# Optimization experiments

Measured on AMD Instinct MI355X. Metric: run time of the kernel, lower is better.

The kernel has to match this reference:

```python
import jax, jax.numpy as jnp
import numpy as np

D = 512          # hidden_dim
H_HEADS = 8
DH = D // H_HEADS  # 64
L = 6            # n_layers
P = 8            # patch size
KT = 3           # temporal kernel
Z_DIM = 32
FILM_SCALE = 0.5
ROPE_BASE = 10000.0
EPS = 1e-5


def layer_norm(x, g, b):
    mu = x.mean(-1, keepdims=True)
    var = ((x - mu) ** 2).mean(-1, keepdims=True)
    return (x - mu) * jax.lax.rsqrt(var + EPS) * g + b


def rotate_half(x):
    x1, x2 = jnp.split(x, 2, axis=-1)
    return jnp.concatenate([-x2, x1], axis=-1)


def rope_time(T, dtype):
    half = DH // 2
    inv_freq = ROPE_BASE ** (-(jnp.arange(half, dtype=dtype) / half))  # (half,)
    angles = jnp.arange(T, dtype=dtype)[:, None] * inv_freq[None, :]   # (T, half)
    sin = jnp.concatenate([jnp.sin(angles), jnp.sin(angles)], -1)      # (T, DH)
    cos = jnp.concatenate([jnp.cos(angles), jnp.cos(angles)], -1)
    return sin, cos


def setup_inputs() -> dict:
    key = jax.random.key(0)
    ks = iter(jax.random.split(key, 64))
    n = lambda shape, s=0.02: jax.random.normal(next(ks), shape, jnp.float32) * s
    inp = {
        "x": jax.random.normal(next(ks), (16, 32, 3, 64, 64), jnp.float32),
        "z": jax.random.normal(next(ks), (16, 32, Z_DIM), jnp.float32),
        # tokenizer: CausalConv3d (kt,ph,pw)=(3,8,8), stride (1,8,8)
        "conv_w": n((D, 3, KT, P, P)),
        "conv_b": jnp.zeros((D,), jnp.float32),
        "tok_g": jnp.ones((D,), jnp.float32),
        "tok_b": jnp.zeros((D,), jnp.float32),
        # FiLM from z -> (gamma, beta)
        "film_w": n((Z_DIM, 2 * D)),
        "film_b": jnp.zeros((2 * D,), jnp.float32),
        # transformer blocks (stacked over L)
        "ln1_g": jnp.ones((L, D), jnp.float32), "ln1_b": jnp.zeros((L, D), jnp.float32),
        "kqv_w": n((L, D, 3 * D)), "kqv_b": jnp.zeros((L, 3 * D), jnp.float32),
        "proj_w": n((L, D, D)), "proj_b": jnp.zeros((L, D), jnp.float32),
        "ln2_g": jnp.ones((L, D), jnp.float32), "ln2_b": jnp.zeros((L, D), jnp.float32),
        "mlp_w1": n((L, D, 4 * D)), "mlp_b1": jnp.zeros((L, 4 * D), jnp.float32),
        "mlp_w2": n((L, 4 * D, D)), "mlp_b2": jnp.zeros((L, D), jnp.float32),
        "rs_attn": jnp.full((L,), 0.5, jnp.float32),
        "rs_mlp": jnp.full((L,), 0.5, jnp.float32),
        # scoring head
        "head_g": jnp.ones((D,), jnp.float32), "head_b": jnp.zeros((D,), jnp.float32),
        "head_w": n((D, 1)), "head_bias": jnp.zeros((1,), jnp.float32),
    }
    return inp


def _forward(x, z, conv_w, conv_b, tok_g, tok_b, film_w, film_b,
             ln1_g, ln1_b, kqv_w, kqv_b, proj_w, proj_b, ln2_g, ln2_b,
             mlp_w1, mlp_b1, mlp_w2, mlp_b2, rs_attn, rs_mlp,
             head_g, head_b, head_w, head_bias):
    B, T, C, Himg, Wimg = x.shape
    # ---- SpatialTemporalTokenizer: causal Conv3d (pad time on past only) ----
    xc = jnp.transpose(x, (0, 2, 1, 3, 4))  # [B,C,T,H,W]
    y = jax.lax.conv_general_dilated(
        xc, conv_w, window_strides=(1, P, P),
        padding=[(KT - 1, 0), (0, 0), (0, 0)],
        dimension_numbers=("NCDHW", "OIDHW", "NCDHW"))
    y = y + conv_b[None, :, None, None, None]          # [B,D,T,Hn,Wn]
    Hn, Wn = y.shape[3], y.shape[4]
    tok = jnp.transpose(y, (0, 2, 3, 4, 1)).reshape(B, T, Hn * Wn, D)
    tok = layer_norm(tok, tok_g, tok_b)                 # [B,T,N,D]
    # ---- FiLM conditioning from z ----
    gb = z @ film_w + film_b                            # [B,T,2D]
    gamma, beta = jnp.split(gb, 2, axis=-1)
    tok = (1.0 + FILM_SCALE * gamma)[:, :, None, :] * tok + (FILM_SCALE * beta)[:, :, None, :]
    # ---- spatial pooling -> temporal sequence ----
    h = tok.mean(axis=2)                                # [B,T,D]
    # ---- transformer stack (causal, time RoPE, pre-LN, gated residuals) ----
    sin_t, cos_t = rope_time(T, h.dtype)                # (T, DH)
    causal = jnp.tril(jnp.ones((T, T), bool))
    neg_inf = jnp.finfo(h.dtype).min
    for i in range(L):
        xi = layer_norm(h, ln1_g[i], ln1_b[i])
        kqv = xi @ kqv_w[i] + kqv_b[i]                  # [B,T,3D]
        k, q, v = jnp.split(kqv, 3, axis=-1)            # torch chunk order: k,q,v
        sh = lambda t: t.reshape(B, T, H_HEADS, DH).transpose(0, 2, 1, 3)  # [B,h,T,d]
        q, k, v = sh(q), sh(k), sh(v)
        q = q * cos_t + rotate_half(q) * sin_t
        k = k * cos_t + rotate_half(k) * sin_t
        att = jnp.einsum("bhqd,bhkd->bhqk", q, k) / np.sqrt(DH)
        att = jnp.where(causal[None, None], att, neg_inf)
        att = jax.nn.softmax(att, axis=-1)
        yv = jnp.einsum("bhqk,bhkd->bhqd", att, v)
        yv = yv.transpose(0, 2, 1, 3).reshape(B, T, D)
        attn_out = yv @ proj_w[i] + proj_b[i]
        h = h + rs_attn[i] * attn_out
        x2 = layer_norm(h, ln2_g[i], ln2_b[i])
        m = jax.nn.gelu(x2 @ mlp_w1[i] + mlp_b1[i], approximate=False) @ mlp_w2[i] + mlp_b2[i]
        h = h + rs_mlp[i] * m
    # ---- per-timestep score head ----
    h = layer_norm(h, head_g, head_b)
    score = (h @ head_w + head_bias)[..., 0]            # [B,T]
    return score


def reference(x, z, conv_w, conv_b, tok_g, tok_b, film_w, film_b,
              ln1_g, ln1_b, kqv_w, kqv_b, proj_w, proj_b, ln2_g, ln2_b,
              mlp_w1, mlp_b1, mlp_w2, mlp_b2, rs_attn, rs_mlp,
              head_g, head_b, head_w, head_bias):
    return _forward(x, z, conv_w, conv_b, tok_g, tok_b, film_w, film_b,
                    ln1_g, ln1_b, kqv_w, kqv_b, proj_w, proj_b, ln2_g, ln2_b,
                    mlp_w1, mlp_b1, mlp_w2, mlp_b2, rs_attn, rs_mlp,
                    head_g, head_b, head_w, head_bias)
```

## Files before the change

### kernel.cpp

```cpp
#include <hip/hip_runtime.h>
#include <math.h>

#define EPS 1e-5f

typedef __attribute__((ext_vector_type(8))) short short8;
typedef __attribute__((ext_vector_type(4))) float f32x4;

__device__ __forceinline__ short f2bf(float f) {
    unsigned u = __float_as_uint(f);
    u += 0x7fffu + ((u >> 16) & 1u);
    return (short)(u >> 16);
}
__device__ __forceinline__ float bf2f(short s) {
    return __uint_as_float(((unsigned)(unsigned short)s) << 16);
}
__device__ __forceinline__ void async16(const void* g, void* l) {
    __builtin_amdgcn_global_load_lds(
        (const __attribute__((address_space(1))) unsigned*)g,
        (__attribute__((address_space(3))) unsigned*)l, 16, 0, 0);
}

__device__ __forceinline__ float block_reduce_sum_256(float v, float* red) {
    #pragma unroll
    for (int o = 32; o > 0; o >>= 1) v += __shfl_down(v, o, 64);
    __syncthreads();
    if ((threadIdx.x & 63) == 0) red[threadIdx.x >> 6] = v;
    __syncthreads();
    return red[0] + red[1] + red[2] + red[3];
}

__global__ __launch_bounds__(256) void prep_all(
    const float* __restrict__ z, const float* __restrict__ fw,
    const float* __restrict__ fb, float* __restrict__ gb,
    const float* __restrict__ conv_w, short* __restrict__ wbf,
    const float* __restrict__ x, short* __restrict__ xbf,
    float* __restrict__ ropeS, float* __restrict__ ropeC,
    const float* __restrict__ kqv_w, short* __restrict__ kqvT,
    const float* __restrict__ proj_w, short* __restrict__ projT,
    const float* __restrict__ mlp_w1, short* __restrict__ mlp1T,
    const float* __restrict__ mlp_w2, short* __restrict__ mlp2T) {
    int bi = blockIdx.x, tid = threadIdx.x;
    if (bi < 512) {
        __shared__ float zs[32];
        if (tid < 32) zs[tid] = z[bi * 32 + tid];
        __syncthreads();
        for (int j = tid; j < 1024; j += 256) {
            float acc = fb[j];
            #pragma unroll
            for (int k = 0; k < 32; k++) acc = fmaf(zs[k], fw[k * 1024 + j], acc);
            gb[bi * 1024 + j] = acc;
        }
        return;
    }
    if (bi < 1664) {
        int i = (bi - 512) * 256 + tid;
        wbf[i] = f2bf(conv_w[i]);
        return;
    }
    if (bi < 4736) {
        int i = (bi - 1664) * 256 + tid;
        float4 a = *(const float4*)(x + (size_t)i * 8);
        float4 b = *(const float4*)(x + (size_t)i * 8 + 4);
        short8 o = {f2bf(a.x), f2bf(a.y), f2bf(a.z), f2bf(a.w),
                    f2bf(b.x), f2bf(b.y), f2bf(b.z), f2bf(b.w)};
        *(short8*)(xbf + (size_t)i * 8) = o;
        return;
    }
    if (bi < 4740) {
        int idx = (bi - 4736) * 256 + tid;
        if (idx < 1024) {
            int t = idx >> 5, j = idx & 31;
            float ang = (float)t * expf(-(float)j * (logf(10000.f) / 32.f));
            ropeS[idx] = sinf(ang);
            ropeC[idx] = cosf(ang);
        }
        return;
    }
    __shared__ float tile[32][33];
    int rel0 = bi - 4740;
    const float* src; short* dst; int NT, K, N, rel;
    if (rel0 < 4608)       { src = kqv_w;  dst = kqvT;  NT = 48; K = 512;  N = 1536; rel = rel0; }
    else if (rel0 < 6144)  { src = proj_w; dst = projT; NT = 16; K = 512;  N = 512;  rel = rel0 - 4608; }
    else if (rel0 < 12288) { src = mlp_w1; dst = mlp1T; NT = 64; K = 512;  N = 2048; rel = rel0 - 6144; }
    else                   { src = mlp_w2; dst = mlp2T; NT = 16; K = 2048; N = 512;  rel = rel0 - 12288; }
    int per = NT * (K / 32);
    int layer = rel / per, r2 = rel - layer * per;
    int nt = r2 % NT, kt = r2 / NT;
    src += (size_t)layer * K * N;
    dst += (size_t)layer * N * K;
    int n0 = nt * 32, k0 = kt * 32;
    int lx = tid & 31, ly = tid >> 5;
    #pragma unroll
    for (int i = 0; i < 32; i += 8)
        tile[ly + i][lx] = src[(size_t)(k0 + ly + i) * N + n0 + lx];
    __syncthreads();
    int kp = tid & 15, nn = tid >> 4;
    #pragma unroll
    for (int i = 0; i < 2; i++) {
        int row = nn + i * 16;
        short2 o = {f2bf(tile[kp * 2][row]), f2bf(tile[kp * 2 + 1][row])};
        *(short2*)(dst + (size_t)(n0 + row) * K + k0 + kp * 2) = o;
    }
}

__global__ __launch_bounds__(256, 2) void conv_fused(
    const short* __restrict__ xbf, const short* __restrict__ wbf,
    const float* __restrict__ cb, const float* __restrict__ tg,
    const float* __restrict__ tb, const float* __restrict__ gb,
    float* __restrict__ h) {
    __shared__ short As[64 * 32];
    __shared__ short Bs[512 * 32];
    __shared__ float redsum[4][64], redss[4][64];
    __shared__ float mu_s[64], inv_s[64];
    int bt = blockIdx.x, b = bt >> 5, t = bt & 31;
    int tid = threadIdx.x;
    int wave = tid >> 6, lane = tid & 63, quad = lane >> 4, l16 = lane & 15;

    int rowA = tid >> 2;
    int cA = (tid & 3) ^ ((rowA >> 1) & 3);
    int hn = rowA >> 3, wn2 = rowA & 7;
    long long baseA = (((long long)(b * 32 + t - 2) * 3) << 12)
                      + (long long)(hn * 8) * 64 + wn2 * 8;

    f32x4 acc[4][8];
    #pragma unroll
    for (int mt = 0; mt < 4; mt++)
        #pragma unroll
        for (int nt = 0; nt < 8; nt++) acc[mt][nt] = (f32x4){0.f, 0.f, 0.f, 0.f};

    for (int k0 = 0; k0 < 576; k0 += 32) {
        #pragma unroll
        for (int e = 0; e < 8; e++) {
            int s = e * 256 + tid;
            int n = s >> 2;
            int c = (s & 3) ^ ((n >> 1) & 3);
            async16(wbf + (size_t)n * 576 + k0 + c * 8, Bs + s * 8);
        }
        {
            int ks = (k0 >> 3) + cA;
            int ch = (ks >= 24) + (ks >= 48);
            int r = ks - ch * 24;
            int kt = r >> 3, ph = r & 7;
            short8 v8 = (short8){0, 0, 0, 0, 0, 0, 0, 0};
            if (t + kt >= 2)
                v8 = *(const short8*)(xbf + baseA
                        + ((long long)(kt * 3 + ch) << 12) + ph * 64);
            *(short8*)(As + tid * 8) = v8;
        }
        __syncthreads();
        short8 af[4], bf[8];
        #pragma unroll
        for (int mt = 0; mt < 4; mt++) {
            int row = mt * 16 + l16;
            int pc = quad ^ ((row >> 1) & 3);
            af[mt] = *(const short8*)(As + row * 32 + pc * 8);
        }
        #pragma unroll
        for (int nt = 0; nt < 8; nt++) {
            int row = wave * 128 + nt * 16 + l16;
            int pc = quad ^ ((row >> 1) & 3);
            bf[nt] = *(const short8*)(Bs + row * 32 + pc * 8);
        }
        #pragma unroll
        for (int mt = 0; mt < 4; mt++)
            #pragma unroll
            for (int nt = 0; nt < 8; nt++)
                acc[mt][nt] = __builtin_amdgcn_mfma_f32_16x16x32_bf16(
                    af[mt], bf[nt], acc[mt][nt], 0, 0, 0);
        __syncthreads();
    }

    float cbn[8], tgn[8], tbn[8], Gn[8], Ben[8];
    #pragma unroll
    for (int nt = 0; nt < 8; nt++) {
        int n = wave * 128 + nt * 16 + l16;
        cbn[nt] = cb[n]; tgn[nt] = tg[n]; tbn[nt] = tb[n];
        Gn[nt]  = 1.f + 0.5f * gb[bt * 1024 + n];
        Ben[nt] = 0.5f * gb[bt * 1024 + 512 + n];
    }
    #pragma unroll
    for (int mt = 0; mt < 4; mt++)
        #pragma unroll
        for (int reg = 0; reg < 4; reg++) {
            float s = 0.f, ss = 0.f;
            #pragma unroll
            for (int nt = 0; nt < 8; nt++) {
                float v = acc[mt][nt][reg] + cbn[nt];
                s += v; ss += v * v;
            }
            #pragma unroll
            for (int o = 1; o < 16; o <<= 1) {
                s  += __shfl_xor(s, o, 64);
                ss += __shfl_xor(ss, o, 64);
            }
            if (l16 == 0) {
                int m = mt * 16 + quad * 4 + reg;
                redsum[wave][m] = s; redss[wave][m] = ss;
            }
        }
    __syncthreads();
    if (tid < 64) {
        float S  = redsum[0][tid] + redsum[1][tid] + redsum[2][tid] + redsum[3][tid];
        float SS = redss[0][tid] + redss[1][tid] + redss[2][tid] + redss[3][tid];
        float mu = S * (1.f / 512.f);
        float var = SS * (1.f / 512.f) - mu * mu;
        mu_s[tid] = mu; inv_s[tid] = rsqrtf(var + EPS);
    }
    __syncthreads();
    float hacc[8] = {0.f, 0.f, 0.f, 0.f, 0.f, 0.f, 0.f, 0.f};
    #pragma unroll
    for (int mt = 0; mt < 4; mt++)
        #pragma unroll
        for (int reg = 0; reg < 4; reg++) {
            int m = mt * 16 + quad * 4 + reg;
            float mu = mu_s[m], inv = inv_s[m];
            #pragma unroll
            for (int nt = 0; nt < 8; nt++) {
                float v = acc[mt][nt][reg] + cbn[nt];
                hacc[nt] += (v - mu) * inv;
            }
        }
    #pragma unroll
    for (int nt = 0; nt < 8; nt++) {
        hacc[nt] += __shfl_xor(hacc[nt], 16, 64);
        hacc[nt] += __shfl_xor(hacc[nt], 32, 64);
    }
    if (quad == 0)
        #pragma unroll
        for (int nt = 0; nt < 8; nt++) {
            int n = wave * 128 + nt * 16 + l16;
            h[bt * 512 + n] = Gn[nt] * (tgn[nt] * (hacc[nt] * (1.f / 64.f)) + tbn[nt])
                              + Ben[nt];
        }
}

__global__ __launch_bounds__(256) void attn_fused(
    const float* __restrict__ hsrc, const float* __restrict__ lng,
    const float* __restrict__ lnb, const short* __restrict__ Bw,
    const float* __restrict__ bias, const float* __restrict__ ropeS,
    const float* __restrict__ ropeC, short* __restrict__ yv) {
    __shared__ char smem[57344] __attribute__((aligned(16)));
    __shared__ float mu_s[32], inv_s[32];
    short* As = (short*)smem;
    short* Bs = (short*)(smem + 32768);
    float (*qsf)[64] = (float(*)[64])(smem);
    float (*ksf)[64] = (float(*)[64])(smem + 8192);
    short* vT  = (short*)(smem + 16384);
    short* qrb = (short*)(smem + 20480);
    short* krb = (short*)(smem + 24576);
    float (*att)[33] = (float(*)[33])(smem + 28672);
    short* pA  = (short*)(smem + 36864);
    int blk = blockIdx.x, b = blk >> 3, hh = blk & 7;
    int tid = threadIdx.x;
    int m0 = b * 32;
    {
        int row = tid >> 3, l8 = tid & 7;
        const float* hp = hsrc + (size_t)(m0 + row) * 512 + l8 * 64;
        float s = 0.f, ss = 0.f;
        #pragma unroll
        for (int i = 0; i < 16; i++) {
            float4 v = *(const float4*)(hp + i * 4);
            s += v.x + v.y + v.z + v.w;
            ss += v.x * v.x + v.y * v.y + v.z * v.z + v.w * v.w;
        }
        s += __shfl_xor(s, 1, 64); ss += __shfl_xor(ss, 1, 64);
        s += __shfl_xor(s, 2, 64); ss += __shfl_xor(ss, 2, 64);
        s += __shfl_xor(s, 4, 64); ss += __shfl_xor(ss, 4, 64);
        if (l8 == 0) {
            float mu = s * (1.f / 512.f);
            float var = ss * (1.f / 512.f) - mu * mu;
            mu_s[row] = mu;
            inv_s[row] = rsqrtf(var + EPS);
        }
    }
    __syncthreads();
    #pragma unroll
    for (int e = 0; e < 8; e++) {
        int lc = e * 256 + tid;
        int row = lc >> 6, cc = lc & 63;
        float mu = mu_s[row], inv = inv_s[row];
        const float* hp = hsrc + (size_t)(m0 + row) * 512 + cc * 8;
        float4 a = *(const float4*)hp, b2 = *(const float4*)(hp + 4);
        float4 g0 = *(const float4*)(lng + cc * 8), g1 = *(const float4*)(lng + cc * 8 + 4);
        float4 b0 = *(const float4*)(lnb + cc * 8), b1 = *(const float4*)(lnb + cc * 8 + 4);
        short8 o = {f2bf((a.x - mu) * inv * g0.x + b0.x),
                    f2bf((a.y - mu) * inv * g0.y + b0.y),
                    f2bf((a.z - mu) * inv * g0.z + b0.z),
                    f2bf((a.w - mu) * inv * g0.w + b0.w),
                    f2bf((b2.x - mu) * inv * g1.x + b1.x),
                    f2bf((b2.y - mu) * inv * g1.y + b1.y),
                    f2bf((b2.z - mu) * inv * g1.z + b1.z),
                    f2bf((b2.w - mu) * inv * g1.w + b1.w)};
        *(short8*)(As + (row * 64 + (cc ^ (row & 7))) * 8) = o;
    }
    __syncthreads();
    int wave = tid >> 6, lane = tid & 63, quad = lane >> 4, l16 = lane & 15;
    f32x4 acc[2][3];
    #pragma unroll
    for (int m2 = 0; m2 < 2; m2++)
        #pragma unroll
        for (int g = 0; g < 3; g++) acc[m2][g] = (f32x4){0.f, 0.f, 0.f, 0.f};
    for (int k0 = 0; k0 < 512; k0 += 64) {
        #pragma unroll
        for (int e = 0; e < 6; e++) {
            int p = e * 256 + tid;
            int row = p >> 3, seg = (p & 7) ^ (row & 7);
            int n = ((row >> 6) << 9) + hh * 64 + (row & 63);
            async16(Bw + (size_t)n * 512 + k0 + seg * 8, Bs + p * 8);
        }
        __syncthreads();
        #pragma unroll
        for (int ksub = 0; ksub < 2; ksub++) {
            int ccb = ksub * 4 + quad;
            short8 af[2], bf[3];
            #pragma unroll
            for (int m2 = 0; m2 < 2; m2++) {
                int row = m2 * 16 + l16;
                int cc = (k0 >> 3) + ccb;
                af[m2] = *(const short8*)(As + (row * 64 + (cc ^ (row & 7))) * 8);
            }
            #pragma unroll
            for (int g = 0; g < 3; g++) {
                int row = g * 64 + wave * 16 + l16;
                bf[g] = *(const short8*)(Bs + (row * 8 + (ccb ^ (row & 7))) * 8);
            }
            #pragma unroll
            for (int m2 = 0; m2 < 2; m2++)
                #pragma unroll
                for (int g = 0; g < 3; g++)
                    acc[m2][g] = __builtin_amdgcn_mfma_f32_16x16x32_bf16(
                        af[m2], bf[g], acc[m2][g], 0, 0, 0);
        }
        __syncthreads();
    }
    float bb0 = bias[hh * 64 + wave * 16 + l16];
    float bb1 = bias[512 + hh * 64 + wave * 16 + l16];
    float bb2 = bias[1024 + hh * 64 + wave * 16 + l16];
    int dcol = wave * 16 + l16;
    #pragma unroll
    for (int m2 = 0; m2 < 2; m2++)
        #pragma unroll
        for (int reg = 0; reg < 4; reg++) {
            int tkn = m2 * 16 + quad * 4 + reg;
            ksf[tkn][dcol] = acc[m2][0][reg] + bb0;
            qsf[tkn][dcol] = acc[m2][1][reg] + bb1;
            vT[dcol * 32 + (((tkn >> 3) ^ (dcol & 3)) << 3) + (tkn & 7)]
                = f2bf(acc[m2][2][reg] + bb2);
        }
    __syncthreads();
    #pragma unroll
    for (int e = 0; e < 8; e++) {
        int idx = e * 256 + tid;
        int t = idx >> 6, d = idx & 63, j = d & 31;
        float sv = ropeS[t * 32 + j], cv = ropeC[t * 32 + j];
        float qv = qsf[t][d], kv = ksf[t][d];
        float qo = qsf[t][d ^ 32], ko = ksf[t][d ^ 32];
        float rq = (d < 32) ? -qo : qo;
        float rk = (d < 32) ? -ko : ko;
        int addr = t * 64 + (((d >> 3) ^ (t & 7)) << 3) + (d & 7);
        qrb[addr] = f2bf(qv * cv + rq * sv);
        krb[addr] = f2bf(kv * cv + rk * sv);
    }
    __syncthreads();
    int mw = wave & 1, nw = wave >> 1;
    {
        f32x4 sc = (f32x4){0.f, 0.f, 0.f, 0.f};
        #pragma unroll
        for (int kc = 0; kc < 2; kc++) {
            int rq = mw * 16 + l16;
            int rk = nw * 16 + l16;
            short8 aq = *(const short8*)(qrb + rq * 64 + ((((kc << 2) + quad) ^ (rq & 7)) << 3));
            short8 bk = *(const short8*)(krb + rk * 64 + ((((kc << 2) + quad) ^ (rk & 7)) << 3));
            sc = __builtin_amdgcn_mfma_f32_16x16x32_bf16(aq, bk, sc, 0, 0, 0);
        }
        #pragma unroll
        for (int reg = 0; reg < 4; reg++) {
            int qt = mw * 16 + quad * 4 + reg;
            int kt = nw * 16 + l16;
            att[qt][kt] = (kt > qt) ? -1e30f : sc[reg] * 0.125f;
        }
    }
    __syncthreads();
    {
        int row = tid >> 3, g = tid & 7;
        float v0 = att[row][g * 4], v1 = att[row][g * 4 + 1];
        float v2 = att[row][g * 4 + 2], v3 = att[row][g * 4 + 3];
        float mx = fmaxf(fmaxf(v0, v1), fmaxf(v2, v3));
        mx = fmaxf(mx, __shfl_xor(mx, 1, 64));
        mx = fmaxf(mx, __shfl_xor(mx, 2, 64));
        mx = fmaxf(mx, __shfl_xor(mx, 4, 64));
        float e0 = expf(v0 - mx), e1 = expf(v1 - mx);
        float e2 = expf(v2 - mx), e3 = expf(v3 - mx);
        float s = e0 + e1 + e2 + e3;
        s += __shfl_xor(s, 1, 64);
        s += __shfl_xor(s, 2, 64);
        s += __shfl_xor(s, 4, 64);
        float inv = 1.f / s;
        short* pp = pA + row * 32 + g * 4;
        pp[0] = f2bf(e0 * inv); pp[1] = f2bf(e1 * inv);
        pp[2] = f2bf(e2 * inv); pp[3] = f2bf(e3 * inv);
    }
    __syncthreads();
    {
        int rp = mw * 16 + l16;
        short8 ap = *(const short8*)(pA + rp * 32 + quad * 8);
        #pragma unroll
        for (int i = 0; i < 2; i++) {
            int nt = (wave >> 1) * 2 + i;
            int rv = nt * 16 + l16;
            short8 bv = *(const short8*)(vT + rv * 32 + (((quad ^ (rv & 3))) << 3));
            f32x4 o = (f32x4){0.f, 0.f, 0.f, 0.f};
            o = __builtin_amdgcn_mfma_f32_16x16x32_bf16(ap, bv, o, 0, 0, 0);
            #pragma unroll
            for (int reg = 0; reg < 4; reg++) {
                int t = mw * 16 + quad * 4 + reg;
                int d = nt * 16 + l16;
                yv[(size_t)(b * 32 + t) * 512 + hh * 64 + d] = f2bf(o[reg]);
            }
        }
    }
}

__global__ __launch_bounds__(256) void gemm_ln(
    const float* __restrict__ hsrc, const float* __restrict__ lng,
    const float* __restrict__ lnb, const short* __restrict__ Bw,
    const float* __restrict__ bias, int N, int mode,
    float* __restrict__ outf, short* __restrict__ outb) {
    __shared__ short As[32 * 512];
    __shared__ short Bs[128 * 128];
    __shared__ float mu_s[32], inv_s[32];
    int tid = threadIdx.x;
    int m0 = blockIdx.y * 32, n0 = blockIdx.x * 128;
    {
        int row = tid >> 3, l8 = tid & 7;
        const float* hp = hsrc + (size_t)(m0 + row) * 512 + l8 * 64;
        float s = 0.f, ss = 0.f;
        #pragma unroll
        for (int i = 0; i < 16; i++) {
            float4 v = *(const float4*)(hp + i * 4);
            s += v.x + v.y + v.z + v.w;
            ss += v.x * v.x + v.y * v.y + v.z * v.z + v.w * v.w;
        }
        s += __shfl_xor(s, 1, 64); ss += __shfl_xor(ss, 1, 64);
        s += __shfl_xor(s, 2, 64); ss += __shfl_xor(ss, 2, 64);
        s += __shfl_xor(s, 4, 64); ss += __shfl_xor(ss, 4, 64);
        if (l8 == 0) {
            float mu = s * (1.f / 512.f);
            float var = ss * (1.f / 512.f) - mu * mu;
            mu_s[row] = mu;
            inv_s[row] = rsqrtf(var + EPS);
        }
    }
    __syncthreads();
    #pragma unroll
    for (int e = 0; e < 8; e++) {
        int lc = e * 256 + tid;
        int row = lc >> 6, cc = lc & 63;
        float mu = mu_s[row], inv = inv_s[row];
        const float* hp = hsrc + (size_t)(m0 + row) * 512 + cc * 8;
        float4 a = *(const float4*)hp, b = *(const float4*)(hp + 4);
        float4 g0 = *(const float4*)(lng + cc * 8), g1 = *(const float4*)(lng + cc * 8 + 4);
        float4 b0 = *(const float4*)(lnb + cc * 8), b1 = *(const float4*)(lnb + cc * 8 + 4);
        short8 o = {f2bf((a.x - mu) * inv * g0.x + b0.x),
                    f2bf((a.y - mu) * inv * g0.y + b0.y),
                    f2bf((a.z - mu) * inv * g0.z + b0.z),
                    f2bf((a.w - mu) * inv * g0.w + b0.w),
                    f2bf((b.x - mu) * inv * g1.x + b1.x),
                    f2bf((b.y - mu) * inv * g1.y + b1.y),
                    f2bf((b.z - mu) * inv * g1.z + b1.z),
                    f2bf((b.w - mu) * inv * g1.w + b1.w)};
        *(short8*)(As + (row * 64 + (cc ^ (row & 7))) * 8) = o;
    }
    __syncthreads();
    int wave = tid >> 6, lane = tid & 63, quad = lane >> 4, l16 = lane & 15;
    f32x4 acc[2][2];
    #pragma unroll
    for (int a2 = 0; a2 < 2; a2++)
        #pragma unroll
        for (int b2 = 0; b2 < 2; b2++) acc[a2][b2] = (f32x4){0.f, 0.f, 0.f, 0.f};
    for (int k0 = 0; k0 < 512; k0 += 128) {
        #pragma unroll
        for (int e = 0; e < 8; e++) {
            int p = e * 256 + tid;
            int row = p >> 4, seg = (p & 15) ^ (row & 15);
            async16(Bw + (size_t)(n0 + row) * 512 + k0 + seg * 8, Bs + p * 8);
        }
        __syncthreads();
        #pragma unroll
        for (int ksub = 0; ksub < 4; ksub++) {
            int ccb = ksub * 4 + quad;
            short8 af[2], bf[2];
            #pragma unroll
            for (int m2 = 0; m2 < 2; m2++) {
                int row = m2 * 16 + l16;
                int cc = (k0 >> 3) + ccb;
                af[m2] = *(const short8*)(As + (row * 64 + (cc ^ (row & 7))) * 8);
            }
            #pragma unroll
            for (int n2 = 0; n2 < 2; n2++) {
                int row = wave * 32 + n2 * 16 + l16;
                bf[n2] = *(const short8*)(Bs + (row * 16 + (ccb ^ (row & 15))) * 8);
            }
            #pragma unroll
            for (int m2 = 0; m2 < 2; m2++)
                #pragma unroll
                for (int n2 = 0; n2 < 2; n2++)
                    acc[m2][n2] = __builtin_amdgcn_mfma_f32_16x16x32_bf16(
                        af[m2], bf[n2], acc[m2][n2], 0, 0, 0);
        }
        __syncthreads();
    }
    #pragma unroll
    for (int m2 = 0; m2 < 2; m2++)
        #pragma unroll
        for (int n2 = 0; n2 < 2; n2++)
            #pragma unroll
            for (int reg = 0; reg < 4; reg++) {
                int m = m0 + m2 * 16 + quad * 4 + reg;
                int n = n0 + wave * 32 + n2 * 16 + l16;
                float v = acc[m2][n2][reg] + bias[n];
                if (mode == 1) {
                    v = 0.5f * v * (1.f + erff(v * 0.70710678118f));
                    outb[(size_t)m * N + n] = f2bf(v);
                } else {
                    outf[(size_t)m * N + n] = v;
                }
            }
}

__global__ __launch_bounds__(256) void gemm_res(
    const short* __restrict__ Ag, const short* __restrict__ Bw,
    const float* __restrict__ bias, const float* __restrict__ rsPtr,
    float* __restrict__ hm, int K, int Ks) {
    __shared__ short As[32 * 128];
    __shared__ short Bs[64 * 128];
    int tid = threadIdx.x;
    int m0 = blockIdx.y * 32, n0 = blockIdx.x * 64;
    int kbase = blockIdx.z * Ks;
    int wave = tid >> 6, lane = tid & 63, quad = lane >> 4, l16 = lane & 15;
    f32x4 acc[2];
    acc[0] = (f32x4){0.f, 0.f, 0.f, 0.f};
    acc[1] = (f32x4){0.f, 0.f, 0.f, 0.f};
    for (int k0 = kbase; k0 < kbase + Ks; k0 += 128) {
        #pragma unroll
        for (int e = 0; e < 2; e++) {
            int p = e * 256 + tid;
            int row = p >> 4, seg = (p & 15) ^ (row & 15);
            async16(Ag + (size_t)(m0 + row) * K + k0 + seg * 8, As + p * 8);
        }
        #pragma unroll
        for (int e = 0; e < 4; e++) {
            int p = e * 256 + tid;
            int row = p >> 4, seg = (p & 15) ^ (row & 15);
            async16(Bw + (size_t)(n0 + row) * K + k0 + seg * 8, Bs + p * 8);
        }
        __syncthreads();
        #pragma unroll
        for (int ksub = 0; ksub < 4; ksub++) {
            int ccb = ksub * 4 + quad;
            short8 bf;
            {
                int row = wave * 16 + l16;
                bf = *(const short8*)(Bs + (row * 16 + (ccb ^ (row & 15))) * 8);
            }
            #pragma unroll
            for (int m2 = 0; m2 < 2; m2++) {
                int row = m2 * 16 + l16;
                short8 af = *(const short8*)(As + (row * 16 + (ccb ^ (row & 15))) * 8);
                acc[m2] = __builtin_amdgcn_mfma_f32_16x16x32_bf16(af, bf, acc[m2], 0, 0, 0);
            }
        }
        __syncthreads();
    }
    float rsv = *rsPtr;
    bool addb = (blockIdx.z == 0);
    #pragma unroll
    for (int m2 = 0; m2 < 2; m2++)
        #pragma unroll
        for (int reg = 0; reg < 4; reg++) {
            int m = m0 + m2 * 16 + quad * 4 + reg;
            int n = n0 + wave * 16 + l16;
            float v = acc[m2][reg] + (addb ? bias[n] : 0.f);
            atomicAdd(&hm[(size_t)m * 512 + n], rsv * v);
        }
}

__global__ __launch_bounds__(256) void head_kernel(
    const float* __restrict__ h, const float* __restrict__ g,
    const float* __restrict__ bb, const float* __restrict__ w,
    const float* __restrict__ bias0, float* __restrict__ out) {
    __shared__ float red[8];
    int token = blockIdx.x, tid = threadIdx.x;
    float v0 = h[token * 512 + tid], v1 = h[token * 512 + tid + 256];
    float s  = block_reduce_sum_256(v0 + v1, red);
    float ss = block_reduce_sum_256(v0 * v0 + v1 * v1, red);
    float mu = s * (1.f / 512.f);
    float var = ss * (1.f / 512.f) - mu * mu;
    float inv = rsqrtf(var + EPS);
    float n0 = (v0 - mu) * inv * g[tid] + bb[tid];
    float n1 = (v1 - mu) * inv * g[tid + 256] + bb[tid + 256];
    float dot = block_reduce_sum_256(n0 * w[tid] + n1 * w[tid + 256], red);
    if (tid == 0) out[token] = dot + bias0[0];
}

extern "C" void kernel_launch(void* const* d_in, const int* in_sizes, int n_in,
                              void* d_out, int out_size, void* d_ws, size_t ws_size,
                              hipStream_t stream) {
    const float* x       = (const float*)d_in[0];
    const float* z       = (const float*)d_in[1];
    const float* conv_w  = (const float*)d_in[2];
    const float* conv_b  = (const float*)d_in[3];
    const float* tok_g   = (const float*)d_in[4];
    const float* tok_b   = (const float*)d_in[5];
    const float* film_w  = (const float*)d_in[6];
    const float* film_b  = (const float*)d_in[7];
    const float* ln1_g   = (const float*)d_in[8];
    const float* ln1_b   = (const float*)d_in[9];
    const float* kqv_w   = (const float*)d_in[10];
    const float* kqv_b   = (const float*)d_in[11];
    const float* proj_w  = (const float*)d_in[12];
    const float* proj_b  = (const float*)d_in[13];
    const float* ln2_g   = (const float*)d_in[14];
    const float* ln2_b   = (const float*)d_in[15];
    const float* mlp_w1  = (const float*)d_in[16];
    const float* mlp_b1  = (const float*)d_in[17];
    const float* mlp_w2  = (const float*)d_in[18];
    const float* mlp_b2  = (const float*)d_in[19];
    const float* rs_attn = (const float*)d_in[20];
    const float* rs_mlp  = (const float*)d_in[21];
    const float* head_g  = (const float*)d_in[22];
    const float* head_b  = (const float*)d_in[23];
    const float* head_w  = (const float*)d_in[24];
    const float* head_bs = (const float*)d_in[25];
    float* out = (float*)d_out;

    float* ws = (float*)d_ws;
    float* gb    = ws;
    float* h     = gb + 524288;
    float* ropeS = h + 262144;
    float* ropeC = ropeS + 1024;
    short* sb = (short*)(ropeC + 1024);
    short* wbf   = sb;
    short* kqvT  = wbf   + 294912;
    short* projT = kqvT  + 4718592;
    short* mlp1T = projT + 1572864;
    short* mlp2T = mlp1T + 6291456;
    short* yvb   = mlp2T + 6291456;
    short* mbuf  = yvb   + 262144;
    short* xbf   = mbuf  + 1048576;

    prep_all<<<23172, 256, 0, stream>>>(
        z, film_w, film_b, gb, conv_w, wbf, x, xbf, ropeS, ropeC,
        kqv_w, kqvT, proj_w, projT, mlp_w1, mlp1T, mlp_w2, mlp2T);

    conv_fused<<<512, 256, 0, stream>>>(xbf, wbf, conv_b, tok_g, tok_b, gb, h);

    for (int i = 0; i < 6; i++) {
        attn_fused<<<128, 256, 0, stream>>>(
            h, ln1_g + i * 512, ln1_b + i * 512,
            kqvT + (size_t)i * 1536 * 512, kqv_b + i * 1536, ropeS, ropeC, yvb);
        gemm_res<<<dim3(8, 16, 2), 256, 0, stream>>>(
            yvb, projT + (size_t)i * 512 * 512, proj_b + i * 512,
            rs_attn + i, h, 512, 256);
        gemm_ln<<<dim3(16, 16), 256, 0, stream>>>(
            h, ln2_g + i * 512, ln2_b + i * 512,
            mlp1T + (size_t)i * 2048 * 512, mlp_b1 + i * 2048,
            2048, 1, nullptr, mbuf);
        gemm_res<<<dim3(8, 16, 4), 256, 0, stream>>>(
            mbuf, mlp2T + (size_t)i * 512 * 2048, mlp_b2 + i * 512,
            rs_mlp + i, h, 2048, 512);
    }

    head_kernel<<<512, 256, 0, stream>>>(h, head_g, head_b, head_w, head_bs, out);
}
```

Before: 465.6 us.

## Double-buffer weight tiles in attention and residual GEMMs, vectorize transpose stores

Adds double-buffered LDS staging for the B weight tiles in attn_fused (narrower K=32 steps) and for both operands in gemm_res. The next tile's async loads are issued before the current tile's MFMAs, so global latency overlaps compute. The first B tile is now prefetched during the LayerNorm prologue in the attention kernel and in the GEMM+GELU kernel. The weight transpose kernel writes 16-byte short8 stores from half the threads instead of short2 stores. The trade-offs are more LDS per block in gemm_res and twice as many loop iterations in attn_fused. There is also a risk of ordering hazards, because no barrier is visible before the next-buffer write in the gemm_res loop.

After: 466.1 us (median of 2 runs). Within noise of the previous version (+0.1%).

```diff
diff --git a/kernel.cpp b/kernel.cpp
--- a/kernel.cpp
+++ b/kernel.cpp
@@ -94,12 +94,12 @@
     for (int i = 0; i < 32; i += 8)
         tile[ly + i][lx] = src[(size_t)(k0 + ly + i) * N + n0 + lx];
     __syncthreads();
-    int kp = tid & 15, nn = tid >> 4;
-    #pragma unroll
-    for (int i = 0; i < 2; i++) {
-        int row = nn + i * 16;
-        short2 o = {f2bf(tile[kp * 2][row]), f2bf(tile[kp * 2 + 1][row])};
-        *(short2*)(dst + (size_t)(n0 + row) * K + k0 + kp * 2) = o;
+    if (tid < 128) {
+        int row = tid >> 2, c = tid & 3;
+        short8 o;
+        #pragma unroll
+        for (int j = 0; j < 8; j++) o[j] = f2bf(tile[c * 8 + j][row]);
+        *(short8*)(dst + (size_t)(n0 + row) * K + k0 + c * 8) = o;
     }
 }
 
@@ -242,7 +242,7 @@
     __shared__ char smem[57344] __attribute__((aligned(16)));
     __shared__ float mu_s[32], inv_s[32];
     short* As = (short*)smem;
-    short* Bs = (short*)(smem + 32768);
+    short* BsB[2] = {(short*)(smem + 32768), (short*)(smem + 45056)};
     float (*qsf)[64] = (float(*)[64])(smem);
     float (*ksf)[64] = (float(*)[64])(smem + 8192);
     short* vT  = (short*)(smem + 16384);
@@ -272,6 +272,13 @@
             mu_s[row] = mu;
             inv_s[row] = rsqrtf(var + EPS);
         }
+    }
+    #pragma unroll
+    for (int e = 0; e < 3; e++) {
+        int p = e * 256 + tid;
+        int row = p >> 2, seg = (p & 3) ^ ((row >> 1) & 3);
+        int n = ((row >> 6) << 9) + hh * 64 + (row & 63);
+        async16(Bw + (size_t)n * 512 + seg * 8, BsB[0] + p * 8);
     }
     __syncthreads();
     #pragma unroll
@@ -300,37 +307,38 @@
     for (int m2 = 0; m2 < 2; m2++)
         #pragma unroll
         for (int g = 0; g < 3; g++) acc[m2][g] = (f32x4){0.f, 0.f, 0.f, 0.f};
-    for (int k0 = 0; k0 < 512; k0 += 64) {
-        #pragma unroll
-        for (int e = 0; e < 6; e++) {
-            int p = e * 256 + tid;
-            int row = p >> 3, seg = (p & 7) ^ (row & 7);
-            int n = ((row >> 6) << 9) + hh * 64 + (row & 63);
-            async16(Bw + (size_t)n * 512 + k0 + seg * 8, Bs + p * 8);
-        }
-        __syncthreads();
-        #pragma unroll
-        for (int ksub = 0; ksub < 2; ksub++) {
-            int ccb = ksub * 4 + quad;
-            short8 af[2], bf[3];
-            #pragma unroll
-            for (int m2 = 0; m2 < 2; m2++) {
-                int row = m2 * 16 + l16;
-                int cc = (k0 >> 3) + ccb;
-                af[m2] = *(const short8*)(As + (row * 64 + (cc ^ (row & 7))) * 8);
-            }
-            #pragma unroll
-            for (int g = 0; g < 3; g++) {
-                int row = g * 64 + wave * 16 + l16;
-                bf[g] = *(const short8*)(Bs + (row * 8 + (ccb ^ (row & 7))) * 8);
-            }
-            #pragma unroll
-            for (int m2 = 0; m2 < 2; m2++)
-                #pragma unroll
-                for (int g = 0; g < 3; g++)
-                    acc[m2][g] = __builtin_amdgcn_mfma_f32_16x16x32_bf16(
-                        af[m2], bf[g], acc[m2][g], 0, 0, 0);
-        }
+    for (int it = 0; it < 16; it++) {
+        short* Bsc = BsB[it & 1];
+        if (it < 15) {
+            int k0n = (it + 1) * 32;
+            short* Bsn = BsB[(it + 1) & 1];
+            #pragma unroll
+            for (int e = 0; e < 3; e++) {
+                int p = e * 256 + tid;
+                int row = p >> 2, seg = (p & 3) ^ ((row >> 1) & 3);
+                int n = ((row >> 6) << 9) + hh * 64 + (row & 63);
+                async16(Bw + (size_t)n * 512 + k0n + seg * 8, Bsn + p * 8);
+            }
+        }
+        int cc = it * 4 + quad;
+        short8 af[2], bf[3];
+        #pragma unroll
+        for (int m2 = 0; m2 < 2; m2++) {
+            int row = m2 * 16 + l16;
+            af[m2] = *(const short8*)(As + (row * 64 + (cc ^ (row & 7))) * 8);
+        }
+        #pragma unroll
+        for (int g = 0; g < 3; g++) {
+            int row = g * 64 + wave * 16 + l16;
+            int pc = quad ^ ((row >> 1) & 3);
+            bf[g] = *(const short8*)(Bsc + (row * 4 + pc) * 8);
+        }
+        #pragma unroll
+        for (int m2 = 0; m2 < 2; m2++)
+            #pragma unroll
+            for (int g = 0; g < 3; g++)
+                acc[m2][g] = __builtin_amdgcn_mfma_f32_16x16x32_bf16(
+                    af[m2], bf[g], acc[m2][g], 0, 0, 0);
         __syncthreads();
     }
     float bb0 = bias[hh * 64 + wave * 16 + l16];
@@ -451,6 +459,12 @@
             inv_s[row] = rsqrtf(var + EPS);
         }
     }
+    #pragma unroll
+    for (int e = 0; e < 8; e++) {
+        int p = e * 256 + tid;
+        int row = p >> 4, seg = (p & 15) ^ (row & 15);
+        async16(Bw + (size_t)(n0 + row) * 512 + seg * 8, Bs + p * 8);
+    }
     __syncthreads();
     #pragma unroll
     for (int e = 0; e < 8; e++) {
@@ -478,14 +492,8 @@
     for (int a2 = 0; a2 < 2; a2++)
         #pragma unroll
         for (int b2 = 0; b2 < 2; b2++) acc[a2][b2] = (f32x4){0.f, 0.f, 0.f, 0.f};
-    for (int k0 = 0; k0 < 512; k0 += 128) {
-        #pragma unroll
-        for (int e = 0; e < 8; e++) {
-            int p = e * 256 + tid;
-            int row = p >> 4, seg = (p & 15) ^ (row & 15);
-            async16(Bw + (size_t)(n0 + row) * 512 + k0 + seg * 8, Bs + p * 8);
-        }
-        __syncthreads();
+    for (int it = 0; it < 4; it++) {
+        int k0 = it * 128;
         #pragma unroll
         for (int ksub = 0; ksub < 4; ksub++) {
             int ccb = ksub * 4 + quad;
@@ -509,6 +517,16 @@
                         af[m2], bf[n2], acc[m2][n2], 0, 0, 0);
         }
         __syncthreads();
+        if (it < 3) {
+            int k0n = (it + 1) * 128;
+            #pragma unroll
+            for (int e = 0; e < 8; e++) {
+                int p = e * 256 + tid;
+                int row = p >> 4, seg = (p & 15) ^ (row & 15);
+                async16(Bw + (size_t)(n0 + row) * 512 + k0n + seg * 8, Bs + p * 8);
+            }
+            __syncthreads();
+        }
     }
     #pragma unroll
     for (int m2 = 0; m2 < 2; m2++)
@@ -532,41 +550,47 @@
     const short* __restrict__ Ag, const short* __restrict__ Bw,
     const float* __restrict__ bias, const float* __restrict__ rsPtr,
     float* __restrict__ hm, int K, int Ks) {
-    __shared__ short As[32 * 128];
-    __shared__ short Bs[64 * 128];
+    __shared__ short As[2][32 * 128];
+    __shared__ short Bs[2][64 * 128];
     int tid = threadIdx.x;
     int m0 = blockIdx.y * 32, n0 = blockIdx.x * 64;
     int kbase = blockIdx.z * Ks;
     int wave = tid >> 6, lane = tid & 63, quad = lane >> 4, l16 = lane & 15;
+    int nIter = Ks >> 7;
     f32x4 acc[2];
     acc[0] = (f32x4){0.f, 0.f, 0.f, 0.f};
     acc[1] = (f32x4){0.f, 0.f, 0.f, 0.f};
-    for (int k0 = kbase; k0 < kbase + Ks; k0 += 128) {
+    auto stage = [&](int k0, int buf) {
         #pragma unroll
         for (int e = 0; e < 2; e++) {
             int p = e * 256 + tid;
             int row = p >> 4, seg = (p & 15) ^ (row & 15);
-            async16(Ag + (size_t)(m0 + row) * K + k0 + seg * 8, As + p * 8);
+            async16(Ag + (size_t)(m0 + row) * K + k0 + seg * 8, As[buf] + p * 8);
         }
         #pragma unroll
         for (int e = 0; e < 4; e++) {
             int p = e * 256 + tid;
             int row = p >> 4, seg = (p & 15) ^ (row & 15);
-            async16(Bw + (size_t)(n0 + row) * K + k0 + seg * 8, Bs + p * 8);
-        }
-        __syncthreads();
+            async16(Bw + (size_t)(n0 + row) * K + k0 + seg * 8, Bs[buf] + p * 8);
+        }
+    };
+    stage(kbase, 0);
+    __syncthreads();
+    for (int it = 0; it < nIter; it++) {
+        int cur = it & 1;
+        if (it + 1 < nIter) stage(kbase + (it + 1) * 128, cur ^ 1);
         #pragma unroll
         for (int ksub = 0; ksub < 4; ksub++) {
             int ccb = ksub * 4 + quad;
             short8 bf;
             {
                 int row = wave * 16 + l16;
-                bf = *(const short8*)(Bs + (row * 16 + (ccb ^ (row & 15))) * 8);
+                bf = *(const short8*)(Bs[cur] + (row * 16 + (ccb ^ (row & 15))) * 8);
             }
             #pragma unroll
             for (int m2 = 0; m2 < 2; m2++) {
                 int row = m2 * 16 + l16;
-                short8 af = *(const short8*)(As + (row * 16 + (ccb ^ (row & 15))) * 8);
+                short8 af = *(const short8*)(As[cur] + (row * 16 + (ccb ^ (row & 15))) * 8);
                 acc[m2] = __builtin_amdgcn_mfma_f32_16x16x32_bf16(af, bf, acc[m2], 0, 0, 0);
             }
         }
```
